# Kernel optimization log

Measured on AMD Instinct MI355X. Metric: run time of the kernel, lower is better.

The kernel has to match this reference:

```python
import jax, jax.numpy as jnp
import numpy as np
import math

B, S, D, H = 4, 2048, 1024, 16
HD = D // H  # head_dim = 64


def setup_inputs() -> dict:
    key = jax.random.key(0)
    ks = jax.random.split(key, 5)
    x = jax.random.normal(ks[0], (B, S, D), dtype=jnp.float32)
    # causal mask, broadcastable over batch and heads
    mask = jnp.tril(jnp.ones((S, S), dtype=bool))[None, None]
    # Linear params in [in, out] layout (math-equivalent to torch's [out, in])
    w_attn = jax.random.normal(ks[1], (D, 3 * D), dtype=jnp.float32) * (1.0 / math.sqrt(D))
    b_attn = jax.random.normal(ks[2], (3 * D,), dtype=jnp.float32) * 0.02
    w_proj = jax.random.normal(ks[3], (D, D), dtype=jnp.float32) * (1.0 / math.sqrt(D))
    b_proj = jax.random.normal(ks[4], (D,), dtype=jnp.float32) * 0.02
    return {"x": x, "mask": mask, "w_attn": w_attn, "b_attn": b_attn,
            "w_proj": w_proj, "b_proj": b_proj}


def reference(x, mask, w_attn, b_attn, w_proj, b_proj):
    b, s, d = x.shape
    # fused qkv projection, then split heads -> [b, h, s, hd]
    qkv = x @ w_attn + b_attn
    q, k, v = jnp.split(qkv, 3, axis=-1)
    split = lambda t: t.reshape(b, s, H, HD).transpose(0, 2, 1, 3)
    q, k, v = split(q), split(k), split(v)
    # scaled dot-product attention with boolean mask (True = keep)
    scores = jnp.einsum('bhqd,bhkd->bhqk', q, k) / math.sqrt(HD)
    scores = jnp.where(mask, scores, -jnp.inf)
    attn = jax.nn.softmax(scores, axis=-1)  # attn_dropout with p=0 is identity
    out = jnp.einsum('bhqk,bhkd->bhqd', attn, v)
    out = out.transpose(0, 2, 1, 3).reshape(b, s, d)
    # output projection (resid_dropout with p=0 is identity)
    return out @ w_proj + b_proj
```

## Files before the change

kernel.cpp:

```cpp
#include <hip/hip_runtime.h>

typedef unsigned short u16;
typedef __attribute__((ext_vector_type(4))) float floatx4;
typedef __attribute__((ext_vector_type(8))) short shortx8;

#define B_ 4
#define S_ 2048
#define D_ 1024
#define H_ 16
#define HD_ 64

__device__ __forceinline__ float b2f(u16 u) {
    return __uint_as_float(((unsigned int)u) << 16);
}
__device__ __forceinline__ u16 f2b(float f) {
    unsigned int u = __float_as_uint(f);
    u += 0x7fffu + ((u >> 16) & 1u);
    return (u16)(u >> 16);
}
__device__ __forceinline__ unsigned long long pack4(float a, float b, float c, float d) {
    return (unsigned long long)f2b(a) | ((unsigned long long)f2b(b) << 16) |
           ((unsigned long long)f2b(c) << 32) | ((unsigned long long)f2b(d) << 48);
}
__device__ __forceinline__ unsigned int permpk(float a, float b) {
    return __builtin_amdgcn_perm(__float_as_uint(b) + 0x8000u,
                                 __float_as_uint(a) + 0x8000u, 0x07060302u);
}
__device__ __forceinline__ void glds16(const u16* g, u16* l) {
    __builtin_amdgcn_global_load_lds(
        (const __attribute__((address_space(1))) unsigned int*)g,
        (__attribute__((address_space(3))) unsigned int*)l, 16, 0, 0);
}

__global__ void detect_dtype(const unsigned int* __restrict__ x, int* __restrict__ flag) {
    const int l = threadIdx.x;
    int cnt = 0;
    for (int i = l; i < 4096; i += 64) {
        const unsigned int e = (x[i] >> 7) & 0xffu;
        cnt += (e >= 110u && e <= 134u) ? 1 : 0;
    }
#pragma unroll
    for (int d = 1; d < 64; d <<= 1) cnt += __shfl_xor(cnt, d);
    if (l == 0) *flag = (cnt > 2048) ? 1 : 0;
}

__global__ __launch_bounds__(256) void convert_x(const void* __restrict__ xin,
                                                 u16* __restrict__ xb,
                                                 const void* __restrict__ bA,
                                                 const void* __restrict__ bP,
                                                 u16* __restrict__ bAb,
                                                 u16* __restrict__ bPb,
                                                 const int* __restrict__ flag) {
    const int isbf = *flag;
    const size_t i = ((size_t)blockIdx.x * 256 + threadIdx.x) * 8;
    if (isbf) {
        *(uint4*)(xb + i) = *(const uint4*)((const u16*)xin + i);
    } else {
        const float* xf = (const float*)xin;
        float4 a = *(const float4*)(xf + i);
        float4 b = *(const float4*)(xf + i + 4);
        u16 o[8] = {f2b(a.x), f2b(a.y), f2b(a.z), f2b(a.w),
                    f2b(b.x), f2b(b.y), f2b(b.z), f2b(b.w)};
        *(uint4*)(xb + i) = *(uint4*)o;
    }
    if (blockIdx.x == 0) {
        for (int j = threadIdx.x; j < 3072; j += 256)
            bAb[j] = isbf ? ((const u16*)bA)[j] : f2b(((const float*)bA)[j]);
        for (int j = threadIdx.x; j < 1024; j += 256)
            bPb[j] = isbf ? ((const u16*)bP)[j] : f2b(((const float*)bP)[j]);
    }
}

__global__ __launch_bounds__(256) void transpose_both(const void* __restrict__ inA,
                                                      u16* __restrict__ outA,
                                                      const void* __restrict__ inP,
                                                      u16* __restrict__ outP,
                                                      const int* __restrict__ flag) {
    const int isbf = *flag;
    __shared__ u16 tile[32][33];
    const int tx = threadIdx.x & 31;
    const int ty = threadIdx.x >> 5;
    int bxi = blockIdx.x;
    const void* in;
    u16* out;
    int N;
    if (bxi < 96) { in = inA; out = outA; N = 3072; }
    else          { in = inP; out = outP; N = 1024; bxi -= 96; }
    const int K = 1024;
    const int bx = bxi * 32;
    const int by = blockIdx.y * 32;
    if (isbf) {
#pragma unroll
        for (int i = 0; i < 32; i += 8)
            tile[ty + i][tx] = ((const u16*)in)[(size_t)(by + ty + i) * N + bx + tx];
    } else {
#pragma unroll
        for (int i = 0; i < 32; i += 8)
            tile[ty + i][tx] = f2b(((const float*)in)[(size_t)(by + ty + i) * N + bx + tx]);
    }
    __syncthreads();
#pragma unroll
    for (int i = 0; i < 32; i += 8)
        out[(size_t)(bx + ty + i) * K + by + tx] = tile[tx][ty + i];
}

template <int MODE>
__global__ __launch_bounds__(256) void gemm_bt(const u16* __restrict__ A,
                                               const u16* __restrict__ BT,
                                               const u16* __restrict__ bias,
                                               void* __restrict__ outv,
                                               int M, int N, int K,
                                               u16* __restrict__ qws,
                                               u16* __restrict__ kws,
                                               u16* __restrict__ vws,
                                               const int* __restrict__ flag) {
    __shared__ __align__(16) u16 As[2][128 * 32];
    __shared__ __align__(16) u16 Bs[2][128 * 32];

    const int isbf = (MODE == 0) ? *flag : 1;
    const int tid = threadIdx.x;
    const int w = tid >> 6, l = tid & 63;
    const int lane_m = l & 15, quad = l >> 4;
    const int bm = blockIdx.x * 128, bn = blockIdx.y * 128;
    const int wm = (w >> 1) * 64, wn = (w & 1) * 64;

    floatx4 acc[4][4];
#pragma unroll
    for (int i = 0; i < 4; i++)
#pragma unroll
        for (int j = 0; j < 4; j++) acc[i][j] = (floatx4){0.f, 0.f, 0.f, 0.f};

    const int lr = l >> 2, sl = l & 3;
    const int cA = sl ^ ((lr >> 1) & 3);
    const int rb0 = w * 16, rb1 = 64 + w * 16;
    const u16* Arow0 = A + (size_t)(bm + rb0 + lr) * K + cA * 8;
    const u16* Arow1 = A + (size_t)(bm + rb1 + lr) * K + cA * 8;
    const u16* Brow0 = BT + (size_t)(bn + rb0 + lr) * K + cA * 8;
    const u16* Brow1 = BT + (size_t)(bn + rb1 + lr) * K + cA * 8;

    auto stage = [&](int t) {
        const int k0 = t * 32;
        u16* ad = &As[t & 1][0];
        u16* bd = &Bs[t & 1][0];
        glds16(Arow0 + k0, ad + rb0 * 32);
        glds16(Arow1 + k0, ad + rb1 * 32);
        glds16(Brow0 + k0, bd + rb0 * 32);
        glds16(Brow1 + k0, bd + rb1 * 32);
    };

    const int NT = K >> 5;
    stage(0);
    for (int t = 0; t < NT; ++t) {
        __syncthreads();
        if (t + 1 < NT) stage(t + 1);

        const u16* Ac = &As[t & 1][0];
        const u16* Bc = &Bs[t & 1][0];
        shortx8 af[4], bf[4];
#pragma unroll
        for (int mb = 0; mb < 4; mb++) {
            const int r = wm + mb * 16 + lane_m;
            af[mb] = *(const shortx8*)(Ac + r * 32 + (quad ^ ((r >> 1) & 3)) * 8);
        }
#pragma unroll
        for (int nb = 0; nb < 4; nb++) {
            const int r = wn + nb * 16 + lane_m;
            bf[nb] = *(const shortx8*)(Bc + r * 32 + (quad ^ ((r >> 1) & 3)) * 8);
        }
#pragma unroll
        for (int mb = 0; mb < 4; mb++)
#pragma unroll
            for (int nb = 0; nb < 4; nb++)
                acc[mb][nb] = __builtin_amdgcn_mfma_f32_16x16x32_bf16(
                    af[mb], bf[nb], acc[mb][nb], 0, 0, 0);
    }

    const float SCALE_Q = 0.18033688011112042f;

    if (MODE == 1 && (bn >> 10) == 2) {
        __syncthreads();
        u16* ep = (w < 2) ? &As[w][0] : &Bs[w - 2][0];
#pragma unroll
        for (int nb = 0; nb < 4; nb++) {
            const int lhd = nb * 16 + lane_m;
            const float bv = b2f(bias[bn + wn + lhd]);
            const int sw = (lhd & 7) << 3;
#pragma unroll
            for (int mb = 0; mb < 4; mb++) {
                const int o = mb * 16 + quad * 4;
                unsigned long long pk =
                    pack4(acc[mb][nb][0] + bv, acc[mb][nb][1] + bv,
                          acc[mb][nb][2] + bv, acc[mb][nb][3] + bv);
                *(unsigned long long*)(ep + lhd * 64 + (o ^ sw)) = pk;
            }
        }
        __syncthreads();
        const int bI = bm >> 11;
        const int hI = ((bn + wn) >> 6) & 15;
        const int s0 = (bm & 2047) + wm;
        u16* vb0 = vws + (size_t)(bI * 16 + hI) * 64 * 2048;
        const int rr8 = l >> 3, c8 = l & 7;
#pragma unroll
        for (int p = 0; p < 8; p++) {
            const int lhd = p * 8 + rr8;
            uint4 v4 = *(const uint4*)(ep + lhd * 64 + ((c8 << 3) ^ ((lhd & 7) << 3)));
            *(uint4*)(vb0 + (size_t)lhd * 2048 + s0 + c8 * 8) = v4;
        }
    } else {
#pragma unroll
        for (int nb = 0; nb < 4; nb++) {
            const int col = bn + wn + nb * 16 + lane_m;
            const float bv = b2f(bias[col]);
#pragma unroll
            for (int mb = 0; mb < 4; mb++) {
                const int rowb = bm + wm + mb * 16 + quad * 4;
#pragma unroll
                for (int r = 0; r < 4; r++) {
                    float v = acc[mb][nb][r] + bv;
                    const int rr = rowb + r;
                    if (MODE == 0) {
                        if (isbf) ((u16*)outv)[(size_t)rr * N + col] = f2b(v);
                        else ((float*)outv)[(size_t)rr * N + col] = v;
                    } else {
                        const int which = col >> 10;
                        if (which == 0) v *= SCALE_Q;
                        const int h = (col >> 6) & 15;
                        const int hd = col & 63;
                        const int b = rr >> 11, s = rr & 2047;
                        u16* dst = which == 0 ? qws : kws;
                        dst[((size_t)(b * 16 + h) * 2048 + s) * 64 + hd] = f2b(v);
                    }
                }
            }
        }
    }
}

__global__ __launch_bounds__(256) void attn_kernel(const u16* __restrict__ Qg,
                                                   const u16* __restrict__ Kg,
                                                   const u16* __restrict__ Vtg,
                                                   u16* __restrict__ Og) {
    __shared__ __align__(16) u16 Ks[2][64 * 64];
    __shared__ __align__(16) u16 Vs[2][64 * 64];
    __shared__ __align__(16) u16 Ps[4][32 * 72];

    const int tid = threadIdx.x, w = tid >> 6, l = tid & 63;
    const int lane_m = l & 15, quad = l >> 4;
    const int bh = blockIdx.y;
    const u16* qp = Qg + (size_t)bh * S_ * 64;
    const u16* kp = Kg + (size_t)bh * S_ * 64;
    const u16* vtp = Vtg + (size_t)bh * 64 * S_;
    u16* psw = &Ps[w][0];
    const int b = bh >> 4, h = bh & 15;

    const int lr8 = l >> 3, sl8 = l & 7;
    const int cK = sl8 ^ (lr8 & 7);
    const int rb0 = w * 8, rb1 = 32 + w * 8;
    const u16* Kr0 = kp + (size_t)(rb0 + lr8) * 64 + cK * 8;
    const u16* Kr1 = kp + (size_t)(rb1 + lr8) * 64 + cK * 8;
    const u16* Vr0 = vtp + (size_t)(rb0 + lr8) * S_ + cK * 8;
    const u16* Vr1 = vtp + (size_t)(rb1 + lr8) * S_ + cK * 8;

    auto stage = [&](int t) {
        const int k0 = t * 64;
        u16* kd = &Ks[t & 1][0];
        u16* vd = &Vs[t & 1][0];
        glds16(Kr0 + (size_t)k0 * 64, kd + rb0 * 64);
        glds16(Kr1 + (size_t)k0 * 64, kd + rb1 * 64);
        glds16(Vr0 + k0, vd + rb0 * 64);
        glds16(Vr1 + k0, vd + rb1 * 64);
    };

    for (int pass = 0; pass < 2; pass++) {
        const int xm = pass ? (15 - (int)blockIdx.x) : (int)blockIdx.x;
        const int q0 = xm * 128;
        const int qw0 = q0 + w * 32;

        shortx8 qF[2][2];
#pragma unroll
        for (int nb = 0; nb < 2; nb++)
#pragma unroll
            for (int ks = 0; ks < 2; ks++)
                qF[nb][ks] = *(const shortx8*)(qp + (size_t)(qw0 + nb * 16 + lane_m) * 64 +
                                               ks * 32 + quad * 8);

        floatx4 o_acc[4][2];
#pragma unroll
        for (int md = 0; md < 4; md++)
#pragma unroll
            for (int nb = 0; nb < 2; nb++) o_acc[md][nb] = (floatx4){0.f, 0.f, 0.f, 0.f};
        float m_i[2] = {-1e30f, -1e30f}, l_i[2] = {0.f, 0.f};

        const int ntiles = (q0 >> 6) + 2;
        const int myend = qw0 + 31;

        __syncthreads();
        stage(0);
        for (int t = 0; t < ntiles; t++) {
            const int k0 = t * 64;
            __syncthreads();
            if (t + 1 < ntiles) stage(t + 1);

            if (k0 <= myend) {
                const u16* kb = &Ks[t & 1][0];
                const u16* vb = &Vs[t & 1][0];
                floatx4 sc[4][2];
#pragma unroll
                for (int mb = 0; mb < 4; mb++)
#pragma unroll
                    for (int nb = 0; nb < 2; nb++) sc[mb][nb] = (floatx4){0.f, 0.f, 0.f, 0.f};
#pragma unroll
                for (int ks = 0; ks < 2; ks++) {
                    shortx8 kA[4];
#pragma unroll
                    for (int mb = 0; mb < 4; mb++) {
                        const int r = mb * 16 + lane_m;
                        kA[mb] = *(const shortx8*)(kb + r * 64 + (((ks * 4 + quad) ^ (r & 7)) * 8));
                    }
                    __builtin_amdgcn_s_setprio(1);
#pragma unroll
                    for (int mb = 0; mb < 4; mb++)
#pragma unroll
                        for (int nb = 0; nb < 2; nb++)
                            sc[mb][nb] = __builtin_amdgcn_mfma_f32_16x16x32_bf16(
                                kA[mb], qF[nb][ks], sc[mb][nb], 0, 0, 0);
                    __builtin_amdgcn_s_setprio(0);
                }

                const bool maskedTile = (k0 + 63 > qw0);
#pragma unroll
                for (int nb = 0; nb < 2; nb++) {
                    const int qg = qw0 + nb * 16 + lane_m;
                    if (maskedTile) {
#pragma unroll
                        for (int mb = 0; mb < 4; mb++)
#pragma unroll
                            for (int r = 0; r < 4; r++) {
                                const int kvg = k0 + mb * 16 + quad * 4 + r;
                                if (kvg > qg) sc[mb][nb][r] = -1e30f;
                            }
                    }
                    float mloc = -1e30f;
#pragma unroll
                    for (int mb = 0; mb < 4; mb++) {
                        float a = fmaxf(fmaxf(sc[mb][nb][0], sc[mb][nb][1]),
                                        fmaxf(sc[mb][nb][2], sc[mb][nb][3]));
                        mloc = fmaxf(mloc, a);
                    }
                    mloc = fmaxf(mloc, __shfl_xor(mloc, 16));
                    mloc = fmaxf(mloc, __shfl_xor(mloc, 32));
                    float mnew = m_i[nb];
                    if (!__all(mloc <= m_i[nb] + 8.0f)) {
                        mnew = fmaxf(m_i[nb], mloc);
                        const float alpha = __builtin_amdgcn_exp2f(m_i[nb] - mnew);
                        m_i[nb] = mnew;
                        l_i[nb] *= alpha;
#pragma unroll
                        for (int md = 0; md < 4; md++) o_acc[md][nb] *= alpha;
                    }
                    float psum = 0.f;
#pragma unroll
                    for (int mb = 0; mb < 4; mb++) {
                        const float p0 = __builtin_amdgcn_exp2f(sc[mb][nb][0] - mnew);
                        const float p1 = __builtin_amdgcn_exp2f(sc[mb][nb][1] - mnew);
                        const float p2 = __builtin_amdgcn_exp2f(sc[mb][nb][2] - mnew);
                        const float p3 = __builtin_amdgcn_exp2f(sc[mb][nb][3] - mnew);
                        psum += (p0 + p1) + (p2 + p3);
                        uint2 pk = {permpk(p0, p1), permpk(p2, p3)};
                        *(uint2*)(psw + (lane_m + 16 * nb) * 72 + mb * 16 + quad * 4) = pk;
                    }
                    psum += __shfl_xor(psum, 16);
                    psum += __shfl_xor(psum, 32);
                    l_i[nb] += psum;
                }

#pragma unroll
                for (int ks = 0; ks < 2; ks++) {
                    shortx8 vF[4], pF[2];
#pragma unroll
                    for (int md = 0; md < 4; md++) {
                        const int r = md * 16 + lane_m;
                        vF[md] = *(const shortx8*)(vb + r * 64 + (((ks * 4 + quad) ^ (r & 7)) * 8));
                    }
#pragma unroll
                    for (int nb = 0; nb < 2; nb++)
                        pF[nb] = *(const shortx8*)(psw + (lane_m + 16 * nb) * 72 + ks * 32 + quad * 8);
                    __builtin_amdgcn_s_setprio(1);
#pragma unroll
                    for (int md = 0; md < 4; md++)
#pragma unroll
                        for (int nb = 0; nb < 2; nb++)
                            o_acc[md][nb] = __builtin_amdgcn_mfma_f32_16x16x32_bf16(
                                vF[md], pF[nb], o_acc[md][nb], 0, 0, 0);
                    __builtin_amdgcn_s_setprio(0);
                }
            }
        }

#pragma unroll
        for (int nb = 0; nb < 2; nb++) {
            const float inv = 1.0f / l_i[nb];
            const int qg = qw0 + nb * 16 + lane_m;
            const size_t base = ((size_t)b * 2048 + qg) * 1024 + h * 64;
#pragma unroll
            for (int md = 0; md < 4; md++) {
                *(unsigned long long*)(Og + base + md * 16 + quad * 4) =
                    pack4(o_acc[md][nb][0] * inv, o_acc[md][nb][1] * inv,
                          o_acc[md][nb][2] * inv, o_acc[md][nb][3] * inv);
            }
        }
    }
}

extern "C" void kernel_launch(void* const* d_in, const int* in_sizes, int n_in,
                              void* d_out, int out_size, void* d_ws, size_t ws_size,
                              hipStream_t stream) {
    const void* x      = d_in[0];
    const void* w_attn = d_in[2];
    const void* b_attn = d_in[3];
    const void* w_proj = d_in[4];
    const void* b_proj = d_in[5];

    u16* qws = (u16*)d_ws;
    u16* kws = qws + 8388608;
    u16* vws = kws + 8388608;
    u16* xb  = vws + 8388608;
    u16* aws = xb;
    u16* wtA = xb + 8388608;
    u16* wtP = wtA + 3145728;
    u16* bAb = wtP + 1048576;
    u16* bPb = bAb + 3072;
    int* flag = (int*)(bPb + 1024);

    detect_dtype<<<1, 64, 0, stream>>>((const unsigned int*)x, flag);
    convert_x<<<4096, 256, 0, stream>>>(x, xb, b_attn, b_proj, bAb, bPb, flag);
    transpose_both<<<dim3(128, 32), 256, 0, stream>>>(w_attn, wtA, w_proj, wtP, flag);

    gemm_bt<1><<<dim3(8192 / 128, 3072 / 128), 256, 0, stream>>>(
        xb, wtA, bAb, nullptr, 8192, 3072, 1024, qws, kws, vws, flag);

    attn_kernel<<<dim3(8, B_ * H_), 256, 0, stream>>>(qws, kws, vws, aws);

    gemm_bt<0><<<dim3(8192 / 128, 1024 / 128), 256, 0, stream>>>(
        aws, wtP, bPb, d_out, 8192, 1024, 1024, nullptr, nullptr, nullptr, flag);
}
```

Baseline: 308.1 us.

## Split attention work across 8 waves of 16 query rows each

The attention kernel now runs 512 threads per block, with each of 8 waves owning 16 query rows instead of 4 waves owning 32. K/V staging is spread across all 8 waves, and per-wave register state (scores, output accumulators, softmax stats) halves. This aims to raise occupancy and latency hiding. The cost is that each K/V fragment read from LDS now feeds only one query block instead of two, which doubles LDS traffic per MFMA.

```diff
diff --git a/kernel.cpp b/kernel.cpp
--- a/kernel.cpp
+++ b/kernel.cpp
@@ -236,13 +236,13 @@
     }
 }
 
-__global__ __launch_bounds__(256) void attn_kernel(const u16* __restrict__ Qg,
-                                                   const u16* __restrict__ Kg,
-                                                   const u16* __restrict__ Vtg,
-                                                   u16* __restrict__ Og) {
+__global__ __launch_bounds__(512, 4) void attn_kernel(const u16* __restrict__ Qg,
+                                                      const u16* __restrict__ Kg,
+                                                      const u16* __restrict__ Vtg,
+                                                      u16* __restrict__ Og) {
     __shared__ __align__(16) u16 Ks[2][64 * 64];
     __shared__ __align__(16) u16 Vs[2][64 * 64];
-    __shared__ __align__(16) u16 Ps[4][32 * 72];
+    __shared__ __align__(16) u16 Ps[8][16 * 72];
 
     const int tid = threadIdx.x, w = tid >> 6, l = tid & 63;
     const int lane_m = l & 15, quad = l >> 4;
@@ -255,44 +255,33 @@
 
     const int lr8 = l >> 3, sl8 = l & 7;
     const int cK = sl8 ^ (lr8 & 7);
-    const int rb0 = w * 8, rb1 = 32 + w * 8;
-    const u16* Kr0 = kp + (size_t)(rb0 + lr8) * 64 + cK * 8;
-    const u16* Kr1 = kp + (size_t)(rb1 + lr8) * 64 + cK * 8;
-    const u16* Vr0 = vtp + (size_t)(rb0 + lr8) * S_ + cK * 8;
-    const u16* Vr1 = vtp + (size_t)(rb1 + lr8) * S_ + cK * 8;
+    const int rbase = w * 8;
+    const u16* Kr = kp + (size_t)(rbase + lr8) * 64 + cK * 8;
+    const u16* Vr = vtp + (size_t)(rbase + lr8) * S_ + cK * 8;
 
     auto stage = [&](int t) {
         const int k0 = t * 64;
-        u16* kd = &Ks[t & 1][0];
-        u16* vd = &Vs[t & 1][0];
-        glds16(Kr0 + (size_t)k0 * 64, kd + rb0 * 64);
-        glds16(Kr1 + (size_t)k0 * 64, kd + rb1 * 64);
-        glds16(Vr0 + k0, vd + rb0 * 64);
-        glds16(Vr1 + k0, vd + rb1 * 64);
+        glds16(Kr + (size_t)k0 * 64, &Ks[t & 1][0] + rbase * 64);
+        glds16(Vr + k0, &Vs[t & 1][0] + rbase * 64);
     };
 
     for (int pass = 0; pass < 2; pass++) {
         const int xm = pass ? (15 - (int)blockIdx.x) : (int)blockIdx.x;
         const int q0 = xm * 128;
-        const int qw0 = q0 + w * 32;
-
-        shortx8 qF[2][2];
-#pragma unroll
-        for (int nb = 0; nb < 2; nb++)
-#pragma unroll
-            for (int ks = 0; ks < 2; ks++)
-                qF[nb][ks] = *(const shortx8*)(qp + (size_t)(qw0 + nb * 16 + lane_m) * 64 +
-                                               ks * 32 + quad * 8);
-
-        floatx4 o_acc[4][2];
-#pragma unroll
-        for (int md = 0; md < 4; md++)
-#pragma unroll
-            for (int nb = 0; nb < 2; nb++) o_acc[md][nb] = (floatx4){0.f, 0.f, 0.f, 0.f};
-        float m_i[2] = {-1e30f, -1e30f}, l_i[2] = {0.f, 0.f};
+        const int qw0 = q0 + w * 16;
+
+        shortx8 qF[2];
+#pragma unroll
+        for (int ks = 0; ks < 2; ks++)
+            qF[ks] = *(const shortx8*)(qp + (size_t)(qw0 + lane_m) * 64 + ks * 32 + quad * 8);
+
+        floatx4 o_acc[4];
+#pragma unroll
+        for (int md = 0; md < 4; md++) o_acc[md] = (floatx4){0.f, 0.f, 0.f, 0.f};
+        float m_i = -1e30f, l_i = 0.f;
 
         const int ntiles = (q0 >> 6) + 2;
-        const int myend = qw0 + 31;
+        const int myend = qw0 + 15;
 
         __syncthreads();
         stage(0);
@@ -304,11 +293,9 @@
             if (k0 <= myend) {
                 const u16* kb = &Ks[t & 1][0];
                 const u16* vb = &Vs[t & 1][0];
-                floatx4 sc[4][2];
-#pragma unroll
-                for (int mb = 0; mb < 4; mb++)
-#pragma unroll
-                    for (int nb = 0; nb < 2; nb++) sc[mb][nb] = (floatx4){0.f, 0.f, 0.f, 0.f};
+                floatx4 sc[4];
+#pragma unroll
+                for (int mb = 0; mb < 4; mb++) sc[mb] = (floatx4){0.f, 0.f, 0.f, 0.f};
 #pragma unroll
                 for (int ks = 0; ks < 2; ks++) {
                     shortx8 kA[4];
@@ -320,93 +307,82 @@
                     __builtin_amdgcn_s_setprio(1);
 #pragma unroll
                     for (int mb = 0; mb < 4; mb++)
-#pragma unroll
-                        for (int nb = 0; nb < 2; nb++)
-                            sc[mb][nb] = __builtin_amdgcn_mfma_f32_16x16x32_bf16(
-                                kA[mb], qF[nb][ks], sc[mb][nb], 0, 0, 0);
+                        sc[mb] = __builtin_amdgcn_mfma_f32_16x16x32_bf16(
+                            kA[mb], qF[ks], sc[mb], 0, 0, 0);
                     __builtin_amdgcn_s_setprio(0);
                 }
 
-                const bool maskedTile = (k0 + 63 > qw0);
-#pragma unroll
-                for (int nb = 0; nb < 2; nb++) {
-                    const int qg = qw0 + nb * 16 + lane_m;
-                    if (maskedTile) {
-#pragma unroll
-                        for (int mb = 0; mb < 4; mb++)
-#pragma unroll
-                            for (int r = 0; r < 4; r++) {
-                                const int kvg = k0 + mb * 16 + quad * 4 + r;
-                                if (kvg > qg) sc[mb][nb][r] = -1e30f;
-                            }
-                    }
-                    float mloc = -1e30f;
-#pragma unroll
-                    for (int mb = 0; mb < 4; mb++) {
-                        float a = fmaxf(fmaxf(sc[mb][nb][0], sc[mb][nb][1]),
-                                        fmaxf(sc[mb][nb][2], sc[mb][nb][3]));
-                        mloc = fmaxf(mloc, a);
-                    }
-                    mloc = fmaxf(mloc, __shfl_xor(mloc, 16));
-                    mloc = fmaxf(mloc, __shfl_xor(mloc, 32));
-                    float mnew = m_i[nb];
-                    if (!__all(mloc <= m_i[nb] + 8.0f)) {
-                        mnew = fmaxf(m_i[nb], mloc);
-                        const float alpha = __builtin_amdgcn_exp2f(m_i[nb] - mnew);
-                        m_i[nb] = mnew;
-                        l_i[nb] *= alpha;
-#pragma unroll
-                        for (int md = 0; md < 4; md++) o_acc[md][nb] *= alpha;
-                    }
-                    float psum = 0.f;
-#pragma unroll
-                    for (int mb = 0; mb < 4; mb++) {
-                        const float p0 = __builtin_amdgcn_exp2f(sc[mb][nb][0] - mnew);
-                        const float p1 = __builtin_amdgcn_exp2f(sc[mb][nb][1] - mnew);
-                        const float p2 = __builtin_amdgcn_exp2f(sc[mb][nb][2] - mnew);
-                        const float p3 = __builtin_amdgcn_exp2f(sc[mb][nb][3] - mnew);
-                        psum += (p0 + p1) + (p2 + p3);
-                        uint2 pk = {permpk(p0, p1), permpk(p2, p3)};
-                        *(uint2*)(psw + (lane_m + 16 * nb) * 72 + mb * 16 + quad * 4) = pk;
-                    }
-                    psum += __shfl_xor(psum, 16);
-                    psum += __shfl_xor(psum, 32);
-                    l_i[nb] += psum;
-                }
+                const int qg = qw0 + lane_m;
+                if (k0 + 63 > qw0) {
+#pragma unroll
+                    for (int mb = 0; mb < 4; mb++)
+#pragma unroll
+                        for (int r = 0; r < 4; r++) {
+                            const int kvg = k0 + mb * 16 + quad * 4 + r;
+                            if (kvg > qg) sc[mb][r] = -1e30f;
+                        }
+                }
+                float mloc = -1e30f;
+#pragma unroll
+                for (int mb = 0; mb < 4; mb++) {
+                    float a = fmaxf(fmaxf(sc[mb][0], sc[mb][1]),
+                                    fmaxf(sc[mb][2], sc[mb][3]));
+                    mloc = fmaxf(mloc, a);
+                }
+                mloc = fmaxf(mloc, __shfl_xor(mloc, 16));
+                mloc = fmaxf(mloc, __shfl_xor(mloc, 32));
+                float mnew = m_i;
+                if (!__all(mloc <= m_i + 8.0f)) {
+                    mnew = fmaxf(m_i, mloc);
+                    const float alpha = __builtin_amdgcn_exp2f(m_i - mnew);
+                    m_i = mnew;
+                    l_i *= alpha;
+#pragma unroll
+                    for (int md = 0; md < 4; md++) o_acc[md] *= alpha;
+                }
+                float psum = 0.f;
+#pragma unroll
+                for (int mb = 0; mb < 4; mb++) {
+                    const float p0 = __builtin_amdgcn_exp2f(sc[mb][0] - mnew);
+                    const float p1 = __builtin_amdgcn_exp2f(sc[mb][1] - mnew);
+                    const float p2 = __builtin_amdgcn_exp2f(sc[mb][2] - mnew);
+                    const float p3 = __builtin_amdgcn_exp2f(sc[mb][3] - mnew);
+                    psum += (p0 + p1) + (p2 + p3);
+                    uint2 pk = {permpk(p0, p1), permpk(p2, p3)};
+                    *(uint2*)(psw + lane_m * 72 + mb * 16 + quad * 4) = pk;
+                }
+                psum += __shfl_xor(psum, 16);
+                psum += __shfl_xor(psum, 32);
+                l_i += psum;
 
 #pragma unroll
                 for (int ks = 0; ks < 2; ks++) {
-                    shortx8 vF[4], pF[2];
+                    shortx8 vF[4], pF;
 #pragma unroll
                     for (int md = 0; md < 4; md++) {
                         const int r = md * 16 + lane_m;
                         vF[md] = *(const shortx8*)(vb + r * 64 + (((ks * 4 + quad) ^ (r & 7)) * 8));
                     }
-#pragma unroll
-                    for (int nb = 0; nb < 2; nb++)
-                        pF[nb] = *(const shortx8*)(psw + (lane_m + 16 * nb) * 72 + ks * 32 + quad * 8);
+                    pF = *(const shortx8*)(psw + lane_m * 72 + ks * 32 + quad * 8);
                     __builtin_amdgcn_s_setprio(1);
 #pragma unroll
                     for (int md = 0; md < 4; md++)
-#pragma unroll
-                        for (int nb = 0; nb < 2; nb++)
-                            o_acc[md][nb] = __builtin_amdgcn_mfma_f32_16x16x32_bf16(
-                                vF[md], pF[nb], o_acc[md][nb], 0, 0, 0);
+                        o_acc[md] = __builtin_amdgcn_mfma_f32_16x16x32_bf16(
+                            vF[md], pF, o_acc[md], 0, 0, 0);
                     __builtin_amdgcn_s_setprio(0);
                 }
             }
         }
 
-#pragma unroll
-        for (int nb = 0; nb < 2; nb++) {
-            const float inv = 1.0f / l_i[nb];
-            const int qg = qw0 + nb * 16 + lane_m;
+        {
+            const float inv = 1.0f / l_i;
+            const int qg = qw0 + lane_m;
             const size_t base = ((size_t)b * 2048 + qg) * 1024 + h * 64;
 #pragma unroll
             for (int md = 0; md < 4; md++) {
                 *(unsigned long long*)(Og + base + md * 16 + quad * 4) =
-                    pack4(o_acc[md][nb][0] * inv, o_acc[md][nb][1] * inv,
-                          o_acc[md][nb][2] * inv, o_acc[md][nb][3] * inv);
+                    pack4(o_acc[md][0] * inv, o_acc[md][1] * inv,
+                          o_acc[md][2] * inv, o_acc[md][3] * inv);
             }
         }
     }
@@ -439,7 +415,7 @@
     gemm_bt<1><<<dim3(8192 / 128, 3072 / 128), 256, 0, stream>>>(
         xb, wtA, bAb, nullptr, 8192, 3072, 1024, qws, kws, vws, flag);
 
-    attn_kernel<<<dim3(8, B_ * H_), 256, 0, stream>>>(qws, kws, vws, aws);
+    attn_kernel<<<dim3(8, B_ * H_), 512, 0, stream>>>(qws, kws, vws, aws);
 
     gemm_bt<0><<<dim3(8192 / 128, 1024 / 128), 256, 0, stream>>>(
         aws, wtP, bPb, d_out, 8192, 1024, 1024, nullptr, nullptr, nullptr, flag);
```

Result: faster. 292.9 us (-4.9%).
